# Kernel tuning notes

Hardware: AMD Instinct MI355X
Metric: run time of the kernel (lower is better)

The kernel has to match this reference:

```python
import jax, jax.numpy as jnp
import numpy as np

B, T, H, A, E, V = 32, 128, 1024, 1024, 512, 512  # A==H required by the module's cat/Linear shapes


def setup_inputs() -> dict:
    key = jax.random.key(0)
    ks = jax.random.split(key, 13)
    s = 0.02
    return {
        "encoder_outputs": jax.random.normal(ks[0], (B, A, E), jnp.float32),
        "hidden": jax.random.normal(ks[1], (1, B, H), jnp.float32),
        "target_seq": jax.random.normal(ks[2], (B, T, H), jnp.float32),
        "W_att": jax.random.normal(ks[3], (H + A, A), jnp.float32) * s,
        "b_att": jax.random.normal(ks[4], (A,), jnp.float32) * s,
        "W_comb": jax.random.normal(ks[5], (H + E, H), jnp.float32) * s,
        "b_comb": jax.random.normal(ks[6], (H,), jnp.float32) * s,
        "W_ih": jax.random.normal(ks[7], (3 * H, H), jnp.float32) * s,
        "b_ih": jax.random.normal(ks[8], (3 * H,), jnp.float32) * s,
        "W_hh": jax.random.normal(ks[9], (3 * H, H), jnp.float32) * s,
        "b_hh": jax.random.normal(ks[10], (3 * H,), jnp.float32) * s,
        "W_out": jax.random.normal(ks[11], (H, V), jnp.float32) * s,
        "b_out": jax.random.normal(ks[12], (V,), jnp.float32) * s,
    }


def reference(encoder_outputs, hidden, target_seq, W_att, b_att, W_comb, b_comb,
              W_ih, b_ih, W_hh, b_hh, W_out, b_out):
    # Teacher forcing: decoder input at step t is zeros (t=0) then target_seq[:, t-1]
    dec_in = jnp.concatenate([jnp.zeros_like(target_seq[:, :1]), target_seq[:, :-1]], axis=1)  # [B,T,H]
    dec_ts = jnp.swapaxes(dec_in, 0, 1)  # [T,B,H]

    def step(h, dec):  # h: [B,H], dec: [B,H]
        # attention over encoder positions (softmax width A == encoder seq len)
        attn = jax.nn.softmax(jnp.concatenate([dec, h], axis=1) @ W_att + b_att, axis=1)  # [B,A]
        ctx = jnp.einsum('bl,ble->be', attn, encoder_outputs)  # [B,E]
        g = jax.nn.relu(jnp.concatenate([dec, ctx], axis=1) @ W_comb + b_comb)  # [B,H]
        # GRU cell (torch gate order r, z, n)
        gi = g @ W_ih.T + b_ih
        gh = h @ W_hh.T + b_hh
        ir, iz, i_n = jnp.split(gi, 3, axis=1)
        hr, hz, h_n = jnp.split(gh, 3, axis=1)
        r = jax.nn.sigmoid(ir + hr)
        z = jax.nn.sigmoid(iz + hz)
        n = jnp.tanh(i_n + r * h_n)
        h_new = (1.0 - z) * n + z * h
        out_tok = h_new @ W_out + b_out  # [B,V]
        return h_new, out_tok

    h_last, outs = jax.lax.scan(step, hidden[0], dec_ts)  # outs: [T,B,V]
    output_seq = jnp.swapaxes(outs, 0, 1)  # [B,T,V]
    return output_seq, h_last[None]
```

## Files before the change

### kernel.cpp

```cpp
#include <hip/hip_runtime.h>

typedef unsigned short u16;
typedef unsigned int u32;
typedef unsigned long long u64;
typedef short v8s __attribute__((ext_vector_type(8)));
typedef float v4f __attribute__((ext_vector_type(4)));

#define MFMA16(a, b, c) __builtin_amdgcn_mfma_f32_16x16x32_bf16((a), (b), (c), 0, 0, 0)

#define B_ 32
#define T_ 128
#define H_ 1024
#define A_ 1024
#define E_ 512
#define V_ 512
#define NBLK 256
#define NTH 512
#define NSLOT 32
#define ENC_LDS_BYTES 131072
#define SCRATCH_BYTES 28672
#define DSMEM_BYTES (ENC_LDS_BYTES + SCRATCH_BYTES)

__device__ __forceinline__ float b2f(u16 u) {
  union { u32 u; float f; } c; c.u = ((u32)u) << 16; return c.f;
}
__device__ __forceinline__ u16 f2b(float f) {
  union { float f; u32 u; } c; c.f = f;
  u32 x = c.u;
  x += 0x7fffu + ((x >> 16) & 1u);
  return (u16)(x >> 16);
}

__device__ __forceinline__ u32 ato_ld(const u32* p) {
  return __hip_atomic_load(p, __ATOMIC_RELAXED, __HIP_MEMORY_SCOPE_AGENT);
}
__device__ __forceinline__ void ato_st(u32* p, u32 v) {
  __hip_atomic_store(p, v, __ATOMIC_RELAXED, __HIP_MEMORY_SCOPE_AGENT);
}
__device__ __forceinline__ float ato_ldf(const float* p) {
  union { u32 u; float f; } c; c.u = ato_ld((const u32*)p); return c.f;
}
__device__ __forceinline__ void ato_stf(float* p, float v) {
  union { float f; u32 u; } c; c.f = v; ato_st((u32*)p, c.u);
}
__device__ __forceinline__ void ato_addf(float* p, float v) {
  __hip_atomic_fetch_add(p, v, __ATOMIC_RELAXED, __HIP_MEMORY_SCOPE_AGENT);
}
__device__ __forceinline__ v8s ld_frag(const u16* p) {
  u64 a = __hip_atomic_load((const u64*)p, __ATOMIC_RELAXED, __HIP_MEMORY_SCOPE_AGENT);
  u64 b = __hip_atomic_load((const u64*)(p + 4), __ATOMIC_RELAXED, __HIP_MEMORY_SCOPE_AGENT);
  union { u64 q[2]; v8s v; } u; u.q[0] = a; u.q[1] = b; return u.v;
}
__device__ __forceinline__ void ld_g8(const float* gp, const float* bc, v8s& hi, v8s& lo) {
  float v[8];
  #pragma unroll
  for (int i = 0; i < 8; i += 2) {
    u64 q = __hip_atomic_load((const u64*)(gp + i), __ATOMIC_RELAXED, __HIP_MEMORY_SCOPE_AGENT);
    union { u64 q; float f[2]; } c; c.q = q;
    v[i] = c.f[0]; v[i + 1] = c.f[1];
  }
  u16 hh[8], ll[8];
  #pragma unroll
  for (int i = 0; i < 8; ++i) {
    float x = fmaxf(v[i] + bc[i], 0.f);
    u16 a = f2b(x);
    hh[i] = a; ll[i] = f2b(x - b2f(a));
  }
  hi = *(v8s*)hh; lo = *(v8s*)ll;
}

__device__ __forceinline__ void grid_bar(u32* arr, u32 ep) {
  asm volatile("s_waitcnt vmcnt(0)" ::: "memory");
  __syncthreads();
  u32* gen = arr + NBLK * NSLOT;
  if (blockIdx.x == 0) {
    int i = threadIdx.x;
    if (i >= 1 && i < NBLK) {
      while (__hip_atomic_load(arr + i * NSLOT, __ATOMIC_RELAXED, __HIP_MEMORY_SCOPE_AGENT) < ep)
        __builtin_amdgcn_s_sleep(1);
    }
    __syncthreads();
    if (threadIdx.x == 0)
      __hip_atomic_store(gen, ep, __ATOMIC_RELAXED, __HIP_MEMORY_SCOPE_AGENT);
  } else {
    if (threadIdx.x == 0) {
      __hip_atomic_store(arr + blockIdx.x * NSLOT, ep, __ATOMIC_RELAXED, __HIP_MEMORY_SCOPE_AGENT);
      while (__hip_atomic_load(gen, __ATOMIC_RELAXED, __HIP_MEMORY_SCOPE_AGENT) < ep)
        __builtin_amdgcn_s_sleep(1);
    }
    __syncthreads();
  }
  asm volatile("" ::: "memory");
}

__device__ __forceinline__ void gemm_nk(const u16* ah, const u16* al, size_t mstr,
                                        const u16* bp, int nk, v4f& c0, v4f& c1) {
  #pragma unroll 2
  for (int i = 0; i < nk; ++i) {
    v8s b   = *(const v8s*)(bp);
    v8s a0h = *(const v8s*)(ah);
    v8s a1h = *(const v8s*)(ah + mstr);
    v8s a0l = *(const v8s*)(al);
    v8s a1l = *(const v8s*)(al + mstr);
    c0 = MFMA16(a0h, b, c0);
    c1 = MFMA16(a1h, b, c1);
    c0 = MFMA16(a0l, b, c0);
    c1 = MFMA16(a1l, b, c1);
    ah += 32; al += 32; bp += 32;
  }
}
__device__ __forceinline__ void gemm_nk_a(const u16* ah, const u16* al, size_t mstr,
                                          const u16* bp, int nk, v4f& c0, v4f& c1) {
  #pragma unroll 2
  for (int i = 0; i < nk; ++i) {
    v8s b   = *(const v8s*)(bp);
    v8s a0h = ld_frag(ah);
    v8s a1h = ld_frag(ah + mstr);
    v8s a0l = ld_frag(al);
    v8s a1l = ld_frag(al + mstr);
    c0 = MFMA16(a0h, b, c0);
    c1 = MFMA16(a1h, b, c1);
    c0 = MFMA16(a0l, b, c0);
    c1 = MFMA16(a1l, b, c1);
    ah += 32; al += 32; bp += 32;
  }
}

__device__ __forceinline__ void red_store2(float* part, int wv, int lane, v4f c0, v4f c1) {
  float* p = part + (wv * 64 + lane) * 8;
  #pragma unroll
  for (int r = 0; r < 4; ++r) { p[r] = c0[r]; p[4 + r] = c1[r]; }
}
__device__ __forceinline__ float red_sum2(const float* part, int o) {
  int m = o >> 4, n = o & 15;
  int lane = (((m & 15) >> 2) << 4) + n;
  int idx = ((m >> 4) << 2) + (m & 3);
  float s = 0.f;
  #pragma unroll
  for (int w = 0; w < 8; ++w) s += part[(w * 64 + lane) * 8 + idx];
  return s;
}

__global__ void __launch_bounds__(NTH, 1)
dec_persist(const u16* __restrict__ tgt_hi, const u16* __restrict__ tgt_lo,
            const u16* __restrict__ WattT, const u16* __restrict__ Whh_b,
            const u16* __restrict__ Wih_b, const u16* __restrict__ WcombT,
            const u16* __restrict__ Wc_ctx,
            const float* __restrict__ enc_f,
            const float* __restrict__ batt, const float* __restrict__ bcomb,
            const float* __restrict__ bih, const float* __restrict__ bhh,
            float* h, float* logit, float* gh, float* g_acc, float* logit_dec,
            u16* hbf_hi, u16* hbf_lo, u16* hseqb, u32* bar)
{
  const int tid = threadIdx.x;
  const int bid = blockIdx.x;
  const int lane = tid & 63;
  const int wv = tid >> 6;
  const int ln = lane & 15;
  const int kq8 = (lane >> 4) * 8;

  extern __shared__ __align__(16) unsigned char dsm[];
  u16* lds_enc = (u16*)dsm;
  float* scratch = (float*)(dsm + ENC_LDS_BYTES);

  {
    int b = bid >> 3, e0 = (bid & 7) * 64;
    const float* src = enc_f + (size_t)b * A_ * E_ + e0 + (tid & 7) * 8;
    int seg = (tid & 7) * 8;
    for (int i = 0; i < 16; ++i) {
      int row = i * 64 + (tid >> 3);
      const float* sp = src + (size_t)row * E_;
      float4 a = *(const float4*)sp;
      float4 bq = *(const float4*)(sp + 4);
      u16 tmp[8] = {f2b(a.x), f2b(a.y), f2b(a.z), f2b(a.w),
                    f2b(bq.x), f2b(bq.y), f2b(bq.z), f2b(bq.w)};
      *(v8s*)(lds_enc + row * 64 + seg) = *(v8s*)tmp;
    }
  }

  u32 ep = 0;

  for (int t = 0; t < T_; ++t) {
    {
      float* part = scratch;
      v4f c0 = {0.f, 0.f, 0.f, 0.f}, c1 = {0.f, 0.f, 0.f, 0.f};
      if (bid < 64) {
        ato_stf(&g_acc[((t + 1) & 1) * (B_ * H_) + bid * 512 + tid], 0.f);
        int n0 = bid * 16;
        const u16* bp = WattT + (size_t)(n0 + ln) * 2048 + 1024 + wv * 128 + kq8;
        size_t abase = (size_t)ln * H_ + wv * 128 + kq8;
        gemm_nk_a(hbf_hi + abase, hbf_lo + abase, (size_t)16 * H_, bp, 4, c0, c1);
      } else {
        int j0 = (bid - 64) * 16;
        const u16* bp = Whh_b + (size_t)(j0 + ln) * H_ + wv * 128 + kq8;
        size_t abase = (size_t)ln * H_ + wv * 128 + kq8;
        gemm_nk_a(hbf_hi + abase, hbf_lo + abase, (size_t)16 * H_, bp, 4, c0, c1);
      }
      red_store2(part, wv, lane, c0, c1);
      __syncthreads();
      {
        float s = red_sum2(part, tid);
        int m = tid >> 4, n = tid & 15;
        if (bid < 64) {
          int n0 = bid * 16;
          float v = s + ato_ldf(&logit_dec[(t & 1) * (B_ * A_) + m * A_ + n0 + n])
                  + batt[n0 + n];
          ato_stf(&logit[m * A_ + n0 + n], v);
        } else {
          int j0 = (bid - 64) * 16;
          ato_stf(&gh[(size_t)(j0 + n) * 32 + m], s + bhh[j0 + n]);
        }
      }
    }
    grid_bar(bar, ++ep);

    {
      float* p    = scratch;
      float* part = scratch + 1024;
      float* red  = scratch + 5120;
      float* sctx = scratch + 5136;
      int b = bid >> 3, es = bid & 7;
      float v1 = ato_ldf(&logit[b * A_ + tid]);
      float v2 = ato_ldf(&logit[b * A_ + 512 + tid]);
      float mx = fmaxf(v1, v2);
      #pragma unroll
      for (int off = 32; off; off >>= 1) mx = fmaxf(mx, __shfl_xor(mx, off));
      if (lane == 0) red[wv] = mx;
      __syncthreads();
      float mfull = red[0];
      #pragma unroll
      for (int q = 1; q < 8; ++q) mfull = fmaxf(mfull, red[q]);
      float e1 = __expf(v1 - mfull), e2 = __expf(v2 - mfull);
      p[tid] = e1; p[512 + tid] = e2;
      float sm = e1 + e2;
      #pragma unroll
      for (int off = 32; off; off >>= 1) sm += __shfl_xor(sm, off);
      if (lane == 0) red[8 + wv] = sm;
      __syncthreads();
      float ssum = red[8];
      #pragma unroll
      for (int q = 1; q < 8; ++q) ssum += red[8 + q];
      float inv = 1.f / ssum;

      int le = lane & 7, lr = lane >> 3;
      float acc[8] = {0.f, 0.f, 0.f, 0.f, 0.f, 0.f, 0.f, 0.f};
      #pragma unroll 4
      for (int i = 0; i < 16; ++i) {
        int l = i * 64 + wv * 8 + lr;
        v8s w = *(const v8s*)(lds_enc + l * 64 + le * 8);
        float pv = p[l];
        #pragma unroll
        for (int r = 0; r < 8; ++r) acc[r] += pv * b2f((u16)w[r]);
      }
      float* pp = part + ((wv * 8 + lr) * 8 + le) * 8;
      #pragma unroll
      for (int r = 0; r < 8; ++r) pp[r] = acc[r];
      __syncthreads();
      if (tid < 64) {
        int eo = tid >> 3, r = tid & 7;
        float s = 0.f;
        #pragma unroll
        for (int q = 0; q < 64; ++q) s += part[q * 64 + eo * 8 + r];
        sctx[tid] = s * inv;
      }
      __syncthreads();
      {
        const u16* wrow = Wc_ctx + (size_t)(es * 64) * H_ + tid * 2;
        float a0 = 0.f, a1 = 0.f;
        #pragma unroll 4
        for (int e = 0; e < 64; ++e) {
          u32 w = *(const u32*)(wrow + (size_t)e * H_);
          float pv = sctx[e];
          a0 += pv * b2f((u16)w);
          a1 += pv * b2f((u16)(w >> 16));
        }
        float* gp = g_acc + (t & 1) * (B_ * H_) + b * H_ + tid * 2;
        ato_addf(gp, a0);
        ato_addf(gp + 1, a1);
      }
    }
    grid_bar(bar, ++ep);

    {
      if (bid < 64) {
        float* part = scratch;
        float* hx   = scratch + 6144;
        int j0 = bid * 16;
        v4f c00 = {0.f,0.f,0.f,0.f}, c01 = c00, c02 = c00, c10 = c00, c11 = c00, c12 = c00;
        const float* gbase = g_acc + (t & 1) * (B_ * H_);
        int koff = wv * 128 + kq8;
        const u16* bp0 = Wih_b + (size_t)(j0 + ln) * H_ + koff;
        const u16* bp1 = bp0 + (size_t)H_ * H_;
        const u16* bp2 = bp0 + (size_t)2 * H_ * H_;
        #pragma unroll
        for (int i = 0; i < 4; ++i) {
          v8s b0 = *(const v8s*)bp0, b1 = *(const v8s*)bp1, b2 = *(const v8s*)bp2;
          v8s a0h, a0l, a1h, a1l;
          ld_g8(gbase + (size_t)ln * H_ + koff, bcomb + koff, a0h, a0l);
          ld_g8(gbase + (size_t)(ln + 16) * H_ + koff, bcomb + koff, a1h, a1l);
          c00 = MFMA16(a0h, b0, c00); c00 = MFMA16(a0l, b0, c00);
          c01 = MFMA16(a0h, b1, c01); c01 = MFMA16(a0l, b1, c01);
          c02 = MFMA16(a0h, b2, c02); c02 = MFMA16(a0l, b2, c02);
          c10 = MFMA16(a1h, b0, c10); c10 = MFMA16(a1l, b0, c10);
          c11 = MFMA16(a1h, b1, c11); c11 = MFMA16(a1l, b1, c11);
          c12 = MFMA16(a1h, b2, c12); c12 = MFMA16(a1l, b2, c12);
          koff += 32; bp0 += 32; bp1 += 32; bp2 += 32;
        }
        #pragma unroll
        for (int pass = 0; pass < 2; ++pass) {
          float* pp = part + (wv * 64 + lane) * 12;
          if (pass == 0) {
            #pragma unroll
            for (int r = 0; r < 4; ++r) { pp[r] = c00[r]; pp[4 + r] = c01[r]; pp[8 + r] = c02[r]; }
          } else {
            #pragma unroll
            for (int r = 0; r < 4; ++r) { pp[r] = c10[r]; pp[4 + r] = c11[r]; pp[8 + r] = c12[r]; }
          }
          __syncthreads();
          if (tid < 256) {
            int obl = tid >> 4, jj = tid & 15;
            int ob = pass * 16 + obl;
            int j = j0 + jj;
            int lanei = ((obl >> 2) << 4) + jj;
            int rg = obl & 3;
            float ir = 0.f, iz = 0.f, in_ = 0.f;
            #pragma unroll
            for (int w = 0; w < 8; ++w) {
              const float* q = part + (w * 64 + lanei) * 12;
              ir += q[rg]; iz += q[4 + rg]; in_ += q[8 + rg];
            }
            ir += bih[j]; iz += bih[H_ + j]; in_ += bih[2 * H_ + j];
            float hr = ato_ldf(&gh[(size_t)j * 32 + ob]);
            float hz = ato_ldf(&gh[(size_t)(H_ + j) * 32 + ob]);
            float hn = ato_ldf(&gh[(size_t)(2 * H_ + j) * 32 + ob]);
            float r = 1.f / (1.f + __expf(-(ir + hr)));
            float z = 1.f / (1.f + __expf(-(iz + hz)));
            float n = tanhf(in_ + r * hn);
            float ho = h[ob * H_ + j];
            float hnew = (1.f - z) * n + z * ho;
            h[ob * H_ + j] = hnew;
            hx[ob * 16 + jj] = hnew;
          }
          __syncthreads();
        }
        if (tid < 256) {
          int ob2 = tid >> 3, j2 = (tid & 7) * 2;
          float v0 = hx[ob2 * 16 + j2], v1 = hx[ob2 * 16 + j2 + 1];
          u16 h0 = f2b(v0), h1 = f2b(v1);
          u16 l0 = f2b(v0 - b2f(h0)), l1 = f2b(v1 - b2f(h1));
          int idx = ob2 * H_ + j0 + j2;
          u32 hp = (u32)h0 | ((u32)h1 << 16);
          ato_st((u32*)(hbf_hi + idx), hp);
          ato_st((u32*)(hbf_lo + idx), (u32)l0 | ((u32)l1 << 16));
          *(u32*)(hseqb + ((size_t)t * 32 + ob2) * H_ + j0 + j2) = hp;
        }
      } else if (bid < 128) {
        if (t < T_ - 1) {
          float* part = scratch;
          int n0 = (bid - 64) * 16;
          v4f c0 = {0.f, 0.f, 0.f, 0.f}, c1 = {0.f, 0.f, 0.f, 0.f};
          size_t abase = ((size_t)ln * T_ + t) * H_ + wv * 128 + kq8;
          const u16* bp = WattT + (size_t)(n0 + ln) * 2048 + wv * 128 + kq8;
          gemm_nk(tgt_hi + abase, tgt_lo + abase, (size_t)16 * T_ * H_, bp, 4, c0, c1);
          red_store2(part, wv, lane, c0, c1);
          __syncthreads();
          int m = tid >> 4, n = tid & 15;
          ato_stf(&logit_dec[((t + 1) & 1) * (B_ * A_) + m * A_ + n0 + n], red_sum2(part, tid));
        }
      } else if (bid < 192) {
        if (t < T_ - 1) {
          float* part = scratch;
          int n0 = (bid - 128) * 16;
          v4f c0 = {0.f, 0.f, 0.f, 0.f}, c1 = {0.f, 0.f, 0.f, 0.f};
          size_t abase = ((size_t)ln * T_ + t) * H_ + wv * 128 + kq8;
          const u16* bp = WcombT + (size_t)(n0 + ln) * 1536 + wv * 128 + kq8;
          gemm_nk(tgt_hi + abase, tgt_lo + abase, (size_t)16 * T_ * H_, bp, 4, c0, c1);
          red_store2(part, wv, lane, c0, c1);
          __syncthreads();
          int m = tid >> 4, n = tid & 15;
          ato_addf(&g_acc[((t + 1) & 1) * (B_ * H_) + m * H_ + n0 + n], red_sum2(part, tid));
        }
      }
    }
    grid_bar(bar, ++ep);
  }
}

__global__ void __launch_bounds__(256, 2)
out_gemm(const u16* __restrict__ hseqb, const u16* __restrict__ WoutT,
         const float* __restrict__ bout, float* __restrict__ out)
{
  int tid = threadIdx.x, lane = tid & 63, wv = tid >> 6;
  int ln = lane & 15, kq8 = (lane >> 4) * 8;
  int m0 = (blockIdx.x >> 3) * 32;
  int n0 = (blockIdx.x & 7) * 64 + wv * 16;
  v4f c0 = {0.f, 0.f, 0.f, 0.f}, c1 = {0.f, 0.f, 0.f, 0.f};
  const u16* ap = hseqb + (size_t)(m0 + ln) * 1024 + kq8;
  const u16* bp = WoutT + (size_t)(n0 + ln) * 1024 + kq8;
  for (int i = 0; i < 32; ++i) {
    v8s b = *(const v8s*)bp;
    v8s a0 = *(const v8s*)ap;
    v8s a1 = *(const v8s*)(ap + 16 * 1024);
    c0 = MFMA16(a0, b, c0);
    c1 = MFMA16(a1, b, c1);
    ap += 32; bp += 32;
  }
  int v = n0 + ln;
  float bo = bout[v];
  int rbase = (lane >> 4) * 4;
  #pragma unroll
  for (int rg = 0; rg < 4; ++rg) {
    int m = m0 + rbase + rg;
    out[((size_t)(m & 31) * T_ + (m >> 5)) * V_ + v] = c0[rg] + bo;
    int m2 = m + 16;
    out[((size_t)(m2 & 31) * T_ + (m2 >> 5)) * V_ + v] = c1[rg] + bo;
  }
}

__global__ void __launch_bounds__(256)
hlast_copy(const float* __restrict__ h, float* __restrict__ out)
{
  int i = blockIdx.x * 256 + threadIdx.x;
  if (i < B_ * H_) out[(size_t)B_ * T_ * V_ + i] = h[i];
}

__global__ void __launch_bounds__(256)
k_cvt(const float* __restrict__ in, u16* __restrict__ out, int n)
{
  int stride = gridDim.x * 256;
  for (int i = blockIdx.x * 256 + threadIdx.x; i < n; i += stride) out[i] = f2b(in[i]);
}

__global__ void __launch_bounds__(256)
k_cvt_split(const float* __restrict__ in, u16* __restrict__ hi, u16* __restrict__ lo, int n)
{
  int stride = gridDim.x * 256;
  for (int i = blockIdx.x * 256 + threadIdx.x; i < n; i += stride) {
    float x = in[i];
    u16 a = f2b(x);
    hi[i] = a;
    lo[i] = f2b(x - b2f(a));
  }
}

__global__ void __launch_bounds__(256)
k_tr(const float* __restrict__ in, u16* __restrict__ out, int R, int C)
{
  __shared__ float tile[32][33];
  int tc = C >> 5;
  int r0 = (blockIdx.x / tc) << 5, c0 = (blockIdx.x % tc) << 5;
  int tx = threadIdx.x & 31, ty = threadIdx.x >> 5;
  #pragma unroll
  for (int q = 0; q < 4; ++q) {
    int r = ty + q * 8;
    tile[r][tx] = in[(size_t)(r0 + r) * C + c0 + tx];
  }
  __syncthreads();
  #pragma unroll
  for (int q = 0; q < 4; ++q) {
    int r = ty + q * 8;
    out[(size_t)(c0 + r) * R + r0 + tx] = f2b(tile[tx][r]);
  }
}

__global__ void __launch_bounds__(256)
k_init(const float* __restrict__ hidden, float* h, u16* hhi, u16* hlo)
{
  int i = blockIdx.x * 256 + threadIdx.x;
  if (i < B_ * H_) {
    float x = hidden[i];
    h[i] = x;
    u16 a = f2b(x);
    hhi[i] = a;
    hlo[i] = f2b(x - b2f(a));
  }
}

extern "C" void kernel_launch(void* const* d_in, const int* in_sizes, int n_in,
                              void* d_out, int out_size, void* d_ws, size_t ws_size,
                              hipStream_t stream) {
  (void)in_sizes; (void)n_in; (void)out_size; (void)ws_size;
  const float* enc    = (const float*)d_in[0];
  const float* hidden = (const float*)d_in[1];
  const float* tgt    = (const float*)d_in[2];
  const float* Watt   = (const float*)d_in[3];
  const float* batt   = (const float*)d_in[4];
  const float* Wcomb  = (const float*)d_in[5];
  const float* bcomb  = (const float*)d_in[6];
  const float* Wih    = (const float*)d_in[7];
  const float* bih    = (const float*)d_in[8];
  const float* Whh    = (const float*)d_in[9];
  const float* bhh    = (const float*)d_in[10];
  const float* Wout   = (const float*)d_in[11];
  const float* bout   = (const float*)d_in[12];

  size_t off = 0;
  char* base = (char*)d_ws;
  auto alloc = [&](size_t bytes) -> void* {
    void* p = base + off;
    off += (bytes + 255) & ~(size_t)255;
    return p;
  };
  size_t bar_bytes = (size_t)(NBLK * NSLOT + NSLOT) * 4;
  u32*   bar    = (u32*)  alloc(bar_bytes);
  float* h      = (float*)alloc(B_ * H_ * 4);
  float* logit  = (float*)alloc(B_ * A_ * 4);
  float* gh     = (float*)alloc((size_t)3 * H_ * B_ * 4);
  float* g_acc  = (float*)alloc((size_t)2 * B_ * H_ * 4);
  float* logit_dec = (float*)alloc((size_t)2 * B_ * A_ * 4);
  u16*   hbf_hi = (u16*)  alloc(B_ * H_ * 2);
  u16*   hbf_lo = (u16*)  alloc(B_ * H_ * 2);
  u16*   hseqb  = (u16*)  alloc((size_t)T_ * B_ * H_ * 2);
  u16*   tgt_hi = (u16*)  alloc((size_t)B_ * T_ * H_ * 2);
  u16*   tgt_lo = (u16*)  alloc((size_t)B_ * T_ * H_ * 2);
  u16*   WattT  = (u16*)  alloc((size_t)2048 * 1024 * 2);
  u16*   Whh_b  = (u16*)  alloc((size_t)3 * H_ * H_ * 2);
  u16*   Wih_b  = (u16*)  alloc((size_t)3 * H_ * H_ * 2);
  u16*   WcombT = (u16*)  alloc((size_t)1024 * 1536 * 2);
  u16*   Wc_ctx = (u16*)  alloc((size_t)512 * 1024 * 2);
  u16*   WoutT  = (u16*)  alloc((size_t)512 * 1024 * 2);

  hipMemsetAsync(bar, 0, bar_bytes, stream);
  hipMemsetAsync(g_acc, 0, (size_t)2 * B_ * H_ * 4, stream);
  hipMemsetAsync(logit_dec, 0, (size_t)2 * B_ * A_ * 4, stream);

  k_cvt_split<<<2048, 256, 0, stream>>>(tgt, tgt_hi, tgt_lo, B_ * T_ * H_);
  k_cvt<<<2048, 256, 0, stream>>>(Whh, Whh_b, 3 * H_ * H_);
  k_cvt<<<2048, 256, 0, stream>>>(Wih, Wih_b, 3 * H_ * H_);
  k_cvt<<<2048, 256, 0, stream>>>(Wcomb + (size_t)1024 * H_, Wc_ctx, 512 * H_);
  k_tr<<<64 * 32, 256, 0, stream>>>(Watt, WattT, 2048, 1024);
  k_tr<<<48 * 32, 256, 0, stream>>>(Wcomb, WcombT, 1536, 1024);
  k_tr<<<32 * 16, 256, 0, stream>>>(Wout, WoutT, 1024, 512);
  k_init<<<128, 256, 0, stream>>>(hidden, h, hbf_hi, hbf_lo);

  hipFuncSetAttribute((const void*)dec_persist,
                      hipFuncAttributeMaxDynamicSharedMemorySize, DSMEM_BYTES);

  dec_persist<<<NBLK, NTH, DSMEM_BYTES, stream>>>(tgt_hi, tgt_lo, WattT, Whh_b, Wih_b,
                                                  WcombT, Wc_ctx, enc,
                                                  batt, bcomb, bih, bhh,
                                                  h, logit, gh, g_acc, logit_dec,
                                                  hbf_hi, hbf_lo, hseqb, bar);
  out_gemm<<<1024, 256, 0, stream>>>(hseqb, WoutT, bout, (float*)d_out);
  hlast_copy<<<128, 256, 0, stream>>>(h, (float*)d_out);
}
```

Before: 4.399 ms.

## Batch coherent loads, flatten grid barrier, prefold bcomb into accumulator init

Replaces per-fragment relaxed atomic loads with inline global_load_dwordx4 sc1 loads. All loads for a stage are issued up front and waited on once before the MFMA chain, so memory latency overlaps instead of serializing. The two-level master/worker grid barrier becomes a flat barrier where every block polls all slots directly, removing one hop of latency per barrier at the cost of more polling traffic. The bcomb bias is now written into the g_acc accumulator at init and reset time rather than added during conversion, and the gh/h/bias operands for the GRU update are prefetched before the reduction.

```diff
diff --git a/kernel.cpp b/kernel.cpp
--- a/kernel.cpp
+++ b/kernel.cpp
@@ -5,6 +5,7 @@
 typedef unsigned long long u64;
 typedef short v8s __attribute__((ext_vector_type(8)));
 typedef float v4f __attribute__((ext_vector_type(4)));
+typedef int v4i __attribute__((ext_vector_type(4)));
 
 #define MFMA16(a, b, c) __builtin_amdgcn_mfma_f32_16x16x32_bf16((a), (b), (c), 0, 0, 0)
 
@@ -31,40 +32,41 @@
   return (u16)(x >> 16);
 }
 
-__device__ __forceinline__ u32 ato_ld(const u32* p) {
-  return __hip_atomic_load(p, __ATOMIC_RELAXED, __HIP_MEMORY_SCOPE_AGENT);
-}
 __device__ __forceinline__ void ato_st(u32* p, u32 v) {
   __hip_atomic_store(p, v, __ATOMIC_RELAXED, __HIP_MEMORY_SCOPE_AGENT);
 }
-__device__ __forceinline__ float ato_ldf(const float* p) {
-  union { u32 u; float f; } c; c.u = ato_ld((const u32*)p); return c.f;
-}
 __device__ __forceinline__ void ato_stf(float* p, float v) {
   union { float f; u32 u; } c; c.f = v; ato_st((u32*)p, c.u);
 }
 __device__ __forceinline__ void ato_addf(float* p, float v) {
   __hip_atomic_fetch_add(p, v, __ATOMIC_RELAXED, __HIP_MEMORY_SCOPE_AGENT);
 }
-__device__ __forceinline__ v8s ld_frag(const u16* p) {
-  u64 a = __hip_atomic_load((const u64*)p, __ATOMIC_RELAXED, __HIP_MEMORY_SCOPE_AGENT);
-  u64 b = __hip_atomic_load((const u64*)(p + 4), __ATOMIC_RELAXED, __HIP_MEMORY_SCOPE_AGENT);
-  union { u64 q[2]; v8s v; } u; u.q[0] = a; u.q[1] = b; return u.v;
-}
-__device__ __forceinline__ void ld_g8(const float* gp, const float* bc, v8s& hi, v8s& lo) {
-  float v[8];
-  #pragma unroll
-  for (int i = 0; i < 8; i += 2) {
-    u64 q = __hip_atomic_load((const u64*)(gp + i), __ATOMIC_RELAXED, __HIP_MEMORY_SCOPE_AGENT);
-    union { u64 q; float f[2]; } c; c.q = q;
-    v[i] = c.f[0]; v[i + 1] = c.f[1];
-  }
+
+__device__ __forceinline__ v4i ld16_sc1(const void* p) {
+  v4i r;
+  asm volatile("global_load_dwordx4 %0, %1, off sc1" : "=v"(r) : "v"(p));
+  return r;
+}
+__device__ __forceinline__ float ld4_sc1(const void* p) {
+  float r;
+  asm volatile("global_load_dword %0, %1, off sc1" : "=v"(r) : "v"(p));
+  return r;
+}
+__device__ __forceinline__ void wait_vm0() {
+  asm volatile("s_waitcnt vmcnt(0)" ::: "memory");
+  __builtin_amdgcn_sched_barrier(0);
+}
+__device__ __forceinline__ v8s as8(v4i x) { union { v4i a; v8s b; } u; u.a = x; return u.b; }
+__device__ __forceinline__ void cvt8(v4i qa, v4i qb, v8s& hi, v8s& lo) {
+  union { v4i q; float f[4]; } a, b;
+  a.q = qa; b.q = qb;
+  float v[8] = {a.f[0], a.f[1], a.f[2], a.f[3], b.f[0], b.f[1], b.f[2], b.f[3]};
   u16 hh[8], ll[8];
   #pragma unroll
   for (int i = 0; i < 8; ++i) {
-    float x = fmaxf(v[i] + bc[i], 0.f);
-    u16 a = f2b(x);
-    hh[i] = a; ll[i] = f2b(x - b2f(a));
+    float x = fmaxf(v[i], 0.f);
+    u16 hv = f2b(x);
+    hh[i] = hv; ll[i] = f2b(x - b2f(hv));
   }
   hi = *(v8s*)hh; lo = *(v8s*)ll;
 }
@@ -72,24 +74,13 @@
 __device__ __forceinline__ void grid_bar(u32* arr, u32 ep) {
   asm volatile("s_waitcnt vmcnt(0)" ::: "memory");
   __syncthreads();
-  u32* gen = arr + NBLK * NSLOT;
-  if (blockIdx.x == 0) {
-    int i = threadIdx.x;
-    if (i >= 1 && i < NBLK) {
-      while (__hip_atomic_load(arr + i * NSLOT, __ATOMIC_RELAXED, __HIP_MEMORY_SCOPE_AGENT) < ep)
-        __builtin_amdgcn_s_sleep(1);
-    }
-    __syncthreads();
-    if (threadIdx.x == 0)
-      __hip_atomic_store(gen, ep, __ATOMIC_RELAXED, __HIP_MEMORY_SCOPE_AGENT);
-  } else {
-    if (threadIdx.x == 0) {
-      __hip_atomic_store(arr + blockIdx.x * NSLOT, ep, __ATOMIC_RELAXED, __HIP_MEMORY_SCOPE_AGENT);
-      while (__hip_atomic_load(gen, __ATOMIC_RELAXED, __HIP_MEMORY_SCOPE_AGENT) < ep)
-        __builtin_amdgcn_s_sleep(1);
-    }
-    __syncthreads();
-  }
+  if (threadIdx.x == 0)
+    __hip_atomic_store(arr + blockIdx.x * NSLOT, ep, __ATOMIC_RELAXED, __HIP_MEMORY_SCOPE_AGENT);
+  if (threadIdx.x < NBLK) {
+    while (__hip_atomic_load(arr + threadIdx.x * NSLOT, __ATOMIC_RELAXED, __HIP_MEMORY_SCOPE_AGENT) < ep)
+      __builtin_amdgcn_s_sleep(1);
+  }
+  __syncthreads();
   asm volatile("" ::: "memory");
 }
 
@@ -109,22 +100,6 @@
     ah += 32; al += 32; bp += 32;
   }
 }
-__device__ __forceinline__ void gemm_nk_a(const u16* ah, const u16* al, size_t mstr,
-                                          const u16* bp, int nk, v4f& c0, v4f& c1) {
-  #pragma unroll 2
-  for (int i = 0; i < nk; ++i) {
-    v8s b   = *(const v8s*)(bp);
-    v8s a0h = ld_frag(ah);
-    v8s a1h = ld_frag(ah + mstr);
-    v8s a0l = ld_frag(al);
-    v8s a1l = ld_frag(al + mstr);
-    c0 = MFMA16(a0h, b, c0);
-    c1 = MFMA16(a1h, b, c1);
-    c0 = MFMA16(a0l, b, c0);
-    c1 = MFMA16(a1l, b, c1);
-    ah += 32; al += 32; bp += 32;
-  }
-}
 
 __device__ __forceinline__ void red_store2(float* part, int wv, int lane, v4f c0, v4f c1) {
   float* p = part + (wv * 64 + lane) * 8;
@@ -183,18 +158,39 @@
   for (int t = 0; t < T_; ++t) {
     {
       float* part = scratch;
+      size_t a0 = (size_t)ln * H_ + wv * 128 + kq8;
+      v4i ah0[4], ah1[4], al0[4], al1[4];
+      #pragma unroll
+      for (int i = 0; i < 4; ++i) {
+        ah0[i] = ld16_sc1(hbf_hi + a0 + i * 32);
+        ah1[i] = ld16_sc1(hbf_hi + a0 + 16 * H_ + i * 32);
+        al0[i] = ld16_sc1(hbf_lo + a0 + i * 32);
+        al1[i] = ld16_sc1(hbf_lo + a0 + 16 * H_ + i * 32);
+      }
+      float ldec = 0.f;
+      const u16* bp;
+      int n0;
+      if (bid < 64) {
+        int gi = bid * 512 + tid;
+        ato_stf(&g_acc[((t + 1) & 1) * (B_ * H_) + gi], bcomb[gi & (H_ - 1)]);
+        n0 = bid * 16;
+        ldec = ld4_sc1(&logit_dec[(t & 1) * (B_ * A_) + (tid >> 4) * A_ + n0 + (tid & 15)]);
+        bp = WattT + (size_t)(n0 + ln) * 2048 + 1024 + wv * 128 + kq8;
+      } else {
+        n0 = (bid - 64) * 16;
+        bp = Whh_b + (size_t)(n0 + ln) * H_ + wv * 128 + kq8;
+      }
+      v8s wb[4];
+      #pragma unroll
+      for (int i = 0; i < 4; ++i) wb[i] = *(const v8s*)(bp + i * 32);
       v4f c0 = {0.f, 0.f, 0.f, 0.f}, c1 = {0.f, 0.f, 0.f, 0.f};
-      if (bid < 64) {
-        ato_stf(&g_acc[((t + 1) & 1) * (B_ * H_) + bid * 512 + tid], 0.f);
-        int n0 = bid * 16;
-        const u16* bp = WattT + (size_t)(n0 + ln) * 2048 + 1024 + wv * 128 + kq8;
-        size_t abase = (size_t)ln * H_ + wv * 128 + kq8;
-        gemm_nk_a(hbf_hi + abase, hbf_lo + abase, (size_t)16 * H_, bp, 4, c0, c1);
-      } else {
-        int j0 = (bid - 64) * 16;
-        const u16* bp = Whh_b + (size_t)(j0 + ln) * H_ + wv * 128 + kq8;
-        size_t abase = (size_t)ln * H_ + wv * 128 + kq8;
-        gemm_nk_a(hbf_hi + abase, hbf_lo + abase, (size_t)16 * H_, bp, 4, c0, c1);
+      wait_vm0();
+      #pragma unroll
+      for (int i = 0; i < 4; ++i) {
+        c0 = MFMA16(as8(ah0[i]), wb[i], c0);
+        c1 = MFMA16(as8(ah1[i]), wb[i], c1);
+        c0 = MFMA16(as8(al0[i]), wb[i], c0);
+        c1 = MFMA16(as8(al1[i]), wb[i], c1);
       }
       red_store2(part, wv, lane, c0, c1);
       __syncthreads();
@@ -202,13 +198,9 @@
         float s = red_sum2(part, tid);
         int m = tid >> 4, n = tid & 15;
         if (bid < 64) {
-          int n0 = bid * 16;
-          float v = s + ato_ldf(&logit_dec[(t & 1) * (B_ * A_) + m * A_ + n0 + n])
-                  + batt[n0 + n];
-          ato_stf(&logit[m * A_ + n0 + n], v);
+          ato_stf(&logit[m * A_ + n0 + n], s + ldec + batt[n0 + n]);
         } else {
-          int j0 = (bid - 64) * 16;
-          ato_stf(&gh[(size_t)(j0 + n) * 32 + m], s + bhh[j0 + n]);
+          ato_stf(&gh[(size_t)(n0 + n) * 32 + m], s + bhh[n0 + n]);
         }
       }
     }
@@ -220,8 +212,9 @@
       float* red  = scratch + 5120;
       float* sctx = scratch + 5136;
       int b = bid >> 3, es = bid & 7;
-      float v1 = ato_ldf(&logit[b * A_ + tid]);
-      float v2 = ato_ldf(&logit[b * A_ + 512 + tid]);
+      float v1 = ld4_sc1(&logit[b * A_ + tid]);
+      float v2 = ld4_sc1(&logit[b * A_ + 512 + tid]);
+      wait_vm0();
       float mx = fmaxf(v1, v2);
       #pragma unroll
       for (int off = 32; off; off >>= 1) mx = fmaxf(mx, __shfl_xor(mx, off));
@@ -286,25 +279,58 @@
         float* part = scratch;
         float* hx   = scratch + 6144;
         int j0 = bid * 16;
-        v4f c00 = {0.f,0.f,0.f,0.f}, c01 = c00, c02 = c00, c10 = c00, c11 = c00, c12 = c00;
         const float* gbase = g_acc + (t & 1) * (B_ * H_);
-        int koff = wv * 128 + kq8;
-        const u16* bp0 = Wih_b + (size_t)(j0 + ln) * H_ + koff;
+        int koff0 = wv * 128 + kq8;
+        v4i gr0[8], gr1[8];
+        #pragma unroll
+        for (int i = 0; i < 4; ++i) {
+          const float* p0 = gbase + (size_t)ln * H_ + koff0 + i * 32;
+          const float* p1 = gbase + (size_t)(ln + 16) * H_ + koff0 + i * 32;
+          gr0[2 * i]     = ld16_sc1(p0);
+          gr0[2 * i + 1] = ld16_sc1(p0 + 4);
+          gr1[2 * i]     = ld16_sc1(p1);
+          gr1[2 * i + 1] = ld16_sc1(p1 + 4);
+        }
+        const u16* bp0 = Wih_b + (size_t)(j0 + ln) * H_ + koff0;
         const u16* bp1 = bp0 + (size_t)H_ * H_;
         const u16* bp2 = bp0 + (size_t)2 * H_ * H_;
+        v8s wb0[4], wb1[4], wb2[4];
         #pragma unroll
         for (int i = 0; i < 4; ++i) {
-          v8s b0 = *(const v8s*)bp0, b1 = *(const v8s*)bp1, b2 = *(const v8s*)bp2;
+          wb0[i] = *(const v8s*)(bp0 + i * 32);
+          wb1[i] = *(const v8s*)(bp1 + i * 32);
+          wb2[i] = *(const v8s*)(bp2 + i * 32);
+        }
+        v4f c00 = {0.f,0.f,0.f,0.f}, c01 = c00, c02 = c00, c10 = c00, c11 = c00, c12 = c00;
+        wait_vm0();
+        #pragma unroll
+        for (int i = 0; i < 4; ++i) {
           v8s a0h, a0l, a1h, a1l;
-          ld_g8(gbase + (size_t)ln * H_ + koff, bcomb + koff, a0h, a0l);
-          ld_g8(gbase + (size_t)(ln + 16) * H_ + koff, bcomb + koff, a1h, a1l);
-          c00 = MFMA16(a0h, b0, c00); c00 = MFMA16(a0l, b0, c00);
-          c01 = MFMA16(a0h, b1, c01); c01 = MFMA16(a0l, b1, c01);
-          c02 = MFMA16(a0h, b2, c02); c02 = MFMA16(a0l, b2, c02);
-          c10 = MFMA16(a1h, b0, c10); c10 = MFMA16(a1l, b0, c10);
-          c11 = MFMA16(a1h, b1, c11); c11 = MFMA16(a1l, b1, c11);
-          c12 = MFMA16(a1h, b2, c12); c12 = MFMA16(a1l, b2, c12);
-          koff += 32; bp0 += 32; bp1 += 32; bp2 += 32;
+          cvt8(gr0[2 * i], gr0[2 * i + 1], a0h, a0l);
+          cvt8(gr1[2 * i], gr1[2 * i + 1], a1h, a1l);
+          c00 = MFMA16(a0h, wb0[i], c00); c00 = MFMA16(a0l, wb0[i], c00);
+          c01 = MFMA16(a0h, wb1[i], c01); c01 = MFMA16(a0l, wb1[i], c01);
+          c02 = MFMA16(a0h, wb2[i], c02); c02 = MFMA16(a0l, wb2[i], c02);
+          c10 = MFMA16(a1h, wb0[i], c10); c10 = MFMA16(a1l, wb0[i], c10);
+          c11 = MFMA16(a1h, wb1[i], c11); c11 = MFMA16(a1l, wb1[i], c11);
+          c12 = MFMA16(a1h, wb2[i], c12); c12 = MFMA16(a1l, wb2[i], c12);
+        }
+        float hr0 = 0.f, hz0 = 0.f, hn0 = 0.f, hr1 = 0.f, hz1 = 0.f, hn1 = 0.f;
+        float ho0 = 0.f, ho1 = 0.f;
+        int obl = tid >> 4, jj = tid & 15, j = j0 + jj;
+        if (tid < 256) {
+          hr0 = ld4_sc1(&gh[(size_t)j * 32 + obl]);
+          hz0 = ld4_sc1(&gh[(size_t)(H_ + j) * 32 + obl]);
+          hn0 = ld4_sc1(&gh[(size_t)(2 * H_ + j) * 32 + obl]);
+          hr1 = ld4_sc1(&gh[(size_t)j * 32 + 16 + obl]);
+          hz1 = ld4_sc1(&gh[(size_t)(H_ + j) * 32 + 16 + obl]);
+          hn1 = ld4_sc1(&gh[(size_t)(2 * H_ + j) * 32 + 16 + obl]);
+          ho0 = h[obl * H_ + j];
+          ho1 = h[(obl + 16) * H_ + j];
+        }
+        float bi_r = 0.f, bi_z = 0.f, bi_n = 0.f;
+        if (tid < 256) {
+          bi_r = bih[j]; bi_z = bih[H_ + j]; bi_n = bih[2 * H_ + j];
         }
         #pragma unroll
         for (int pass = 0; pass < 2; ++pass) {
@@ -318,9 +344,8 @@
           }
           __syncthreads();
           if (tid < 256) {
-            int obl = tid >> 4, jj = tid & 15;
+            if (pass == 0) wait_vm0();
             int ob = pass * 16 + obl;
-            int j = j0 + jj;
             int lanei = ((obl >> 2) << 4) + jj;
             int rg = obl & 3;
             float ir = 0.f, iz = 0.f, in_ = 0.f;
@@ -329,14 +354,14 @@
               const float* q = part + (w * 64 + lanei) * 12;
               ir += q[rg]; iz += q[4 + rg]; in_ += q[8 + rg];
             }
-            ir += bih[j]; iz += bih[H_ + j]; in_ += bih[2 * H_ + j];
-            float hr = ato_ldf(&gh[(size_t)j * 32 + ob]);
-            float hz = ato_ldf(&gh[(size_t)(H_ + j) * 32 + ob]);
-            float hn = ato_ldf(&gh[(size_t)(2 * H_ + j) * 32 + ob]);
+            ir += bi_r; iz += bi_z; in_ += bi_n;
+            float hr = pass ? hr1 : hr0;
+            float hz = pass ? hz1 : hz0;
+            float hn = pass ? hn1 : hn0;
+            float ho = pass ? ho1 : ho0;
             float r = 1.f / (1.f + __expf(-(ir + hr)));
             float z = 1.f / (1.f + __expf(-(iz + hz)));
             float n = tanhf(in_ + r * hn);
-            float ho = h[ob * H_ + j];
             float hnew = (1.f - z) * n + z * ho;
             h[ob * H_ + j] = hnew;
             hx[ob * 16 + jj] = hnew;
@@ -464,7 +489,8 @@
 }
 
 __global__ void __launch_bounds__(256)
-k_init(const float* __restrict__ hidden, float* h, u16* hhi, u16* hlo)
+k_init(const float* __restrict__ hidden, const float* __restrict__ bcomb,
+       float* h, u16* hhi, u16* hlo, float* g_acc)
 {
   int i = blockIdx.x * 256 + threadIdx.x;
   if (i < B_ * H_) {
@@ -473,6 +499,7 @@
     u16 a = f2b(x);
     hhi[i] = a;
     hlo[i] = f2b(x - b2f(a));
+    g_acc[i] = bcomb[i & (H_ - 1)];
   }
 }
 
@@ -521,7 +548,6 @@
   u16*   WoutT  = (u16*)  alloc((size_t)512 * 1024 * 2);
 
   hipMemsetAsync(bar, 0, bar_bytes, stream);
-  hipMemsetAsync(g_acc, 0, (size_t)2 * B_ * H_ * 4, stream);
   hipMemsetAsync(logit_dec, 0, (size_t)2 * B_ * A_ * 4, stream);
 
   k_cvt_split<<<2048, 256, 0, stream>>>(tgt, tgt_hi, tgt_lo, B_ * T_ * H_);
@@ -531,7 +557,7 @@
   k_tr<<<64 * 32, 256, 0, stream>>>(Watt, WattT, 2048, 1024);
   k_tr<<<48 * 32, 256, 0, stream>>>(Wcomb, WcombT, 1536, 1024);
   k_tr<<<32 * 16, 256, 0, stream>>>(Wout, WoutT, 1024, 512);
-  k_init<<<128, 256, 0, stream>>>(hidden, h, hbf_hi, hbf_lo);
+  k_init<<<128, 256, 0, stream>>>(hidden, bcomb, h, hbf_hi, hbf_lo, g_acc);
 
   hipFuncSetAttribute((const void*)dec_persist,
                       hipFuncAttributeMaxDynamicSharedMemorySize, DSMEM_BYTES);
```

New measurement: 3.641 ms. 17.2% less time.
